# Kernel optimization log

Hardware: AMD Instinct MI355X
Metric: run time of the kernel (lower is better)

## Reference

```python
import jax, jax.numpy as jnp
import numpy as np

SHIFTS = 1
WINDOW_SIZES = (4, 8, 16)
BN_EPS = 1e-5


def _calc_attn_path(x, ws, shifts):
    # x: (b, H, W, 2c) with channels laid out as (qv=2, c)
    b, H, W, c2 = x.shape
    c = c2 // 2
    if shifts > 0:
        x = jnp.roll(x, shift=(-ws // 2, -ws // 2), axis=(1, 2))
    h, w = H // ws, W // ws
    # 'b (h dh) (w dw) (qv c) -> qv (b h w) (dh dw c)'
    qv = x.reshape(b, h, ws, w, ws, 2, c).transpose(5, 0, 1, 3, 2, 4, 6)
    qv = qv.reshape(2, b * h * w, ws * ws * c)
    q, v = qv[0], qv[1]                       # (N, D), N = b*h*w windows, D = ws*ws*c
    atn = jax.nn.softmax(q @ q.T, axis=-1)    # (N, N) attention across windows (as in source)
    y = atn @ v                               # (N, D)
    # '(b h w) (dh dw c) -> b (h dh) (w dw) c'
    y = y.reshape(b, h, w, ws, ws, c).transpose(0, 1, 3, 2, 4, 5).reshape(b, H, W, c)
    if shifts > 0:
        y = jnp.roll(y, shift=(ws // 2, ws // 2), axis=(1, 2))
    return y, atn


def setup_inputs() -> dict:
    key = jax.random.key(0)
    ks = jax.random.split(key, 3)
    B, H, W, C = 4, 128, 128, 180
    inputs = jax.random.normal(ks[0], (B, H, W, C), jnp.float32)
    conv1_w = jax.random.normal(ks[1], (1, 1, C, 2 * C), jnp.float32) * 0.05
    conv1_b = jnp.zeros((2 * C,), jnp.float32)
    bn_scale = jnp.ones((2 * C,), jnp.float32)
    bn_bias = jnp.zeros((2 * C,), jnp.float32)
    conv2_w = jax.random.normal(ks[2], (1, 1, C, C), jnp.float32) * 0.05
    conv2_b = jnp.zeros((C,), jnp.float32)
    return {"inputs": inputs, "conv1_w": conv1_w, "conv1_b": conv1_b,
            "bn_scale": bn_scale, "bn_bias": bn_bias,
            "conv2_w": conv2_w, "conv2_b": conv2_b}


def reference(inputs, conv1_w, conv1_b, bn_scale, bn_bias, conv2_w, conv2_b):
    # 1x1 conv to 2*C channels (calc_attn=True)
    x = jnp.einsum('bhwc,cd->bhwd', inputs, conv1_w[0, 0]) + conv1_b
    # BatchNorm in training mode (batch statistics)
    mean = x.mean(axis=(0, 1, 2))
    var = x.var(axis=(0, 1, 2))
    x = (x - mean) * jax.lax.rsqrt(var + BN_EPS) * bn_scale + bn_bias
    xs = jnp.split(x, 3, axis=-1)             # three groups of 2*C/3 channels
    ys, attns = [], []
    for ws, xi in zip(WINDOW_SIZES, xs):
        y, a = _calc_attn_path(xi, ws, SHIFTS)
        ys.append(y)
        attns.append(a)
    y = jnp.concatenate(ys, axis=-1)          # back to C channels
    y = jnp.einsum('bhwc,cd->bhwd', y, conv2_w[0, 0]) + conv2_b
    return (y, *attns)
```

## Files before the change

kernel.cpp:

```cpp
#include <hip/hip_runtime.h>

typedef unsigned short u16;
typedef __bf16 bf16x8 __attribute__((ext_vector_type(8)));
typedef float f32x4 __attribute__((ext_vector_type(4)));
typedef u16 u16x4 __attribute__((ext_vector_type(4)));
typedef u16 u16x8 __attribute__((ext_vector_type(8)));

__device__ __forceinline__ u16 f2bf(float v) {
    unsigned u = __float_as_uint(v);
    unsigned r = (u + 0x7fffu + ((u >> 16) & 1u)) >> 16;
    return (u16)r;
}
__device__ __forceinline__ float bf2f(u16 u) { return __uint_as_float(((unsigned)u) << 16); }

__device__ __forceinline__ void async_cp16(const u16* g, u16* l) {
    __builtin_amdgcn_global_load_lds((const __attribute__((address_space(1))) unsigned int*)g,
                                     (__attribute__((address_space(3))) unsigned int*)l, 16, 0, 0);
}

__global__ __launch_bounds__(256) void gemm_f32(
    const u16* __restrict__ A, const u16* __restrict__ B,
    float* __restrict__ C, const float* __restrict__ bias,
    int K, int ldc, int n_store)
{
    __shared__ char smem[16384];
    u16* As = (u16*)smem;
    u16* Bs = (u16*)(smem + 8192);
    const int tid = threadIdx.x;
    const int lane = tid & 63;
    const int wave = tid >> 6;
    const int wm = wave >> 1, wn = wave & 1;
    const long m0 = (long)blockIdx.y * 128;
    const long n0 = (long)blockIdx.x * 128;

    f32x4 acc[4][4] = {};
    const int lrow = tid >> 2;
    const int lk = (tid & 3) << 3;
    const u16* Ag = A + (m0 + lrow) * (long)K + lk;
    const u16* Bg = B + (n0 + lrow) * (long)K + lk;
    u16* Asl = As + tid * 8;
    u16* Bsl = Bs + tid * 8;
    const long K64 = (long)64 * K;

    for (int k0 = 0; k0 < K; k0 += 32) {
        async_cp16(Ag + k0, Asl);
        async_cp16(Ag + k0 + K64, Asl + 2048);
        async_cp16(Bg + k0, Bsl);
        async_cp16(Bg + k0 + K64, Bsl + 2048);
        __syncthreads();
        bf16x8 af[4], bg[4];
        const int ro = (lane & 15) * 32 + ((lane >> 4) << 3);
#pragma unroll
        for (int i = 0; i < 4; i++) af[i] = *(const bf16x8*)(As + (wm * 64 + i * 16) * 32 + ro);
#pragma unroll
        for (int j = 0; j < 4; j++) bg[j] = *(const bf16x8*)(Bs + (wn * 64 + j * 16) * 32 + ro);
#pragma unroll
        for (int i = 0; i < 4; i++)
#pragma unroll
            for (int j = 0; j < 4; j++)
                acc[i][j] = __builtin_amdgcn_mfma_f32_16x16x32_bf16(af[i], bg[j], acc[i][j], 0, 0, 0);
        __syncthreads();
    }

    float bv[4];
#pragma unroll
    for (int j = 0; j < 4; j++) bv[j] = bias[n0 + wn * 64 + j * 16 + (lane & 15)];

    float* Cs = (float*)smem;
    for (int c = 0; c < 4; c++) {
        __syncthreads();
        if (wm == (c >> 1)) {
#pragma unroll
            for (int ii = 0; ii < 2; ii++) {
                const int i = (c & 1) * 2 + ii;
#pragma unroll
                for (int j = 0; j < 4; j++)
#pragma unroll
                    for (int r = 0; r < 4; r++) {
                        const int lr = ii * 16 + ((lane >> 4) << 2) + r;
                        Cs[lr * 128 + wn * 64 + j * 16 + (lane & 15)] = acc[i][j][r] + bv[j];
                    }
            }
        }
        __syncthreads();
        const int lr = tid >> 3;
        const int cg = (tid & 7) * 16;
        const long rowg = m0 + c * 32 + lr;
#pragma unroll
        for (int e = 0; e < 4; e++) {
            const int colg = cg + e * 4;
            if ((int)n0 + colg < n_store)
                *(f32x4*)(C + rowg * (long)ldc + n0 + colg) = *(const f32x4*)(Cs + lr * 128 + colg);
        }
    }
}

__global__ __launch_bounds__(256) void conv1_gemm(
    const float* __restrict__ A, const u16* __restrict__ B,
    u16* __restrict__ C, const float* __restrict__ bias)
{
    __shared__ char smem[16384];
    u16* As = (u16*)smem;
    u16* Bs = (u16*)(smem + 8192);
    const int tid = threadIdx.x;
    const int lane = tid & 63;
    const int wave = tid >> 6;
    const int wm = wave >> 1, wn = wave & 1;
    const long m0 = (long)blockIdx.y * 128;
    const long n0 = (long)blockIdx.x * 128;

    f32x4 acc[4][4] = {};
    const int lrow = tid >> 2;
    const int lk = (tid & 3) << 3;
    const float* Ar0 = A + (m0 + lrow) * 180L;
    const float* Ar1 = Ar0 + 64 * 180L;
    const u16* Bg = B + (n0 + lrow) * 192L + lk;
    u16* Asl = As + tid * 8;
    u16* Bsl = Bs + tid * 8;

#pragma unroll
    for (int k0 = 0; k0 < 192; k0 += 32) {
        const int gk = k0 + lk;
        u16x8 oa, ob;
        if (gk + 8 <= 180) {
            f32x4 a0 = *(const f32x4*)(Ar0 + gk), a1 = *(const f32x4*)(Ar0 + gk + 4);
            f32x4 b0 = *(const f32x4*)(Ar1 + gk), b1 = *(const f32x4*)(Ar1 + gk + 4);
#pragma unroll
            for (int c = 0; c < 4; c++) {
                oa[c] = f2bf(a0[c]); oa[4 + c] = f2bf(a1[c]);
                ob[c] = f2bf(b0[c]); ob[4 + c] = f2bf(b1[c]);
            }
        } else if (gk < 180) {
            f32x4 a0 = *(const f32x4*)(Ar0 + gk);
            f32x4 b0 = *(const f32x4*)(Ar1 + gk);
#pragma unroll
            for (int c = 0; c < 4; c++) {
                oa[c] = f2bf(a0[c]); oa[4 + c] = 0;
                ob[c] = f2bf(b0[c]); ob[4 + c] = 0;
            }
        } else {
#pragma unroll
            for (int c = 0; c < 8; c++) { oa[c] = 0; ob[c] = 0; }
        }
        *(u16x8*)Asl = oa;
        *(u16x8*)(Asl + 2048) = ob;
        async_cp16(Bg + k0, Bsl);
        async_cp16(Bg + k0 + 64 * 192, Bsl + 2048);
        __syncthreads();
        bf16x8 af[4], bg[4];
        const int ro = (lane & 15) * 32 + ((lane >> 4) << 3);
#pragma unroll
        for (int i = 0; i < 4; i++) af[i] = *(const bf16x8*)(As + (wm * 64 + i * 16) * 32 + ro);
#pragma unroll
        for (int j = 0; j < 4; j++) bg[j] = *(const bf16x8*)(Bs + (wn * 64 + j * 16) * 32 + ro);
#pragma unroll
        for (int i = 0; i < 4; i++)
#pragma unroll
            for (int j = 0; j < 4; j++)
                acc[i][j] = __builtin_amdgcn_mfma_f32_16x16x32_bf16(af[i], bg[j], acc[i][j], 0, 0, 0);
        __syncthreads();
    }

    float bv[4];
#pragma unroll
    for (int j = 0; j < 4; j++) bv[j] = bias[n0 + wn * 64 + j * 16 + (lane & 15)];

    u16* Cs = (u16*)smem;
    for (int c = 0; c < 2; c++) {
        __syncthreads();
        if (wm == c) {
#pragma unroll
            for (int i = 0; i < 4; i++)
#pragma unroll
                for (int j = 0; j < 4; j++)
#pragma unroll
                    for (int r = 0; r < 4; r++) {
                        const int lr = i * 16 + ((lane >> 4) << 2) + r;
                        Cs[lr * 128 + wn * 64 + j * 16 + (lane & 15)] = f2bf(acc[i][j][r] + bv[j]);
                    }
        }
        __syncthreads();
        const int lr = tid >> 2;
        const int cg = (tid & 3) * 32;
        const long rowg = m0 + c * 64 + lr;
#pragma unroll
        for (int e = 0; e < 4; e++) {
            const int colg = cg + e * 8;
            *(u16x8*)(C + rowg * 384L + n0 + colg) = *(const u16x8*)(Cs + lr * 128 + colg);
        }
    }
}

__global__ __launch_bounds__(256) void qq_all(
    const u16* __restrict__ q0, const u16* __restrict__ q1, const u16* __restrict__ q2,
    float* __restrict__ S0, float* __restrict__ pG1, float* __restrict__ pG2)
{
    __shared__ char smem[16384];
    u16* As = (u16*)smem;
    u16* Bs = (u16*)(smem + 8192);
    const int bid = blockIdx.x;
    int seg, local;
    if (bid < 1024) { seg = 0; local = bid; }
    else if (bid < 1536) { seg = 1; local = bid - 1024; }
    else { seg = 2; local = bid - 1536; }
    const int tX = seg == 0 ? 32 : (seg == 1 ? 8 : 2);
    const int tt = tX * tX;
    const int K = seg == 0 ? 1024 : (seg == 1 ? 3840 : 15360);
    const int Ksplit = seg == 0 ? 1024 : (seg == 1 ? 480 : 256);
    const int N = seg == 0 ? 4096 : (seg == 1 ? 1024 : 256);
    const u16* A = seg == 0 ? q0 : (seg == 1 ? q1 : q2);
    float* outP = seg == 0 ? S0 : (seg == 1 ? pG1 : pG2);
    const int z = local / tt;
    const int rem = local - z * tt;
    const int bx = rem % tX;
    const int by = rem / tX;

    const int tid = threadIdx.x;
    const int lane = tid & 63;
    const int wave = tid >> 6;
    const int wm = wave >> 1, wn = wave & 1;
    const long m0 = (long)by * 128;
    const long n0 = (long)bx * 128;
    const int kbeg = z * Ksplit;

    f32x4 acc[4][4] = {};
    const int lrow = tid >> 2;
    const int lk = (tid & 3) << 3;
    const u16* Ag = A + (m0 + lrow) * (long)K + lk;
    const u16* Bg = A + (n0 + lrow) * (long)K + lk;
    u16* Asl = As + tid * 8;
    u16* Bsl = Bs + tid * 8;
    const long K64 = (long)64 * K;

    for (int k0 = kbeg; k0 < kbeg + Ksplit; k0 += 32) {
        async_cp16(Ag + k0, Asl);
        async_cp16(Ag + k0 + K64, Asl + 2048);
        async_cp16(Bg + k0, Bsl);
        async_cp16(Bg + k0 + K64, Bsl + 2048);
        __syncthreads();
        bf16x8 af[4], bg[4];
        const int ro = (lane & 15) * 32 + ((lane >> 4) << 3);
#pragma unroll
        for (int i = 0; i < 4; i++) af[i] = *(const bf16x8*)(As + (wm * 64 + i * 16) * 32 + ro);
#pragma unroll
        for (int j = 0; j < 4; j++) bg[j] = *(const bf16x8*)(Bs + (wn * 64 + j * 16) * 32 + ro);
#pragma unroll
        for (int i = 0; i < 4; i++)
#pragma unroll
            for (int j = 0; j < 4; j++)
                acc[i][j] = __builtin_amdgcn_mfma_f32_16x16x32_bf16(af[i], bg[j], acc[i][j], 0, 0, 0);
        __syncthreads();
    }

    float* Pz = outP + (long)z * N * N;
    float* Cs = (float*)smem;
    for (int c = 0; c < 4; c++) {
        __syncthreads();
        if (wm == (c >> 1)) {
#pragma unroll
            for (int ii = 0; ii < 2; ii++) {
                const int i = (c & 1) * 2 + ii;
#pragma unroll
                for (int j = 0; j < 4; j++)
#pragma unroll
                    for (int r = 0; r < 4; r++) {
                        const int lr = ii * 16 + ((lane >> 4) << 2) + r;
                        Cs[lr * 128 + wn * 64 + j * 16 + (lane & 15)] = acc[i][j][r];
                    }
            }
        }
        __syncthreads();
        const int lr = tid >> 3;
        const int cg = (tid & 7) * 16;
        const long rowg = m0 + c * 32 + lr;
#pragma unroll
        for (int e = 0; e < 4; e++) {
            const int colg = cg + e * 4;
            *(f32x4*)(Pz + rowg * (long)N + n0 + colg) = *(const f32x4*)(Cs + lr * 128 + colg);
        }
    }
}

__global__ __launch_bounds__(256) void pv_all(
    const u16* __restrict__ a0, const u16* __restrict__ a1, const u16* __restrict__ a2,
    const u16* __restrict__ vt0, const u16* __restrict__ vt1, const u16* __restrict__ vt2,
    u16* __restrict__ Ysp)
{
    __shared__ char smem[16384];
    u16* As = (u16*)smem;
    u16* Bs = (u16*)(smem + 8192);
    const int bid = blockIdx.x;
    int seg, local;
    if (bid < 256) { seg = 0; local = bid; }
    else if (bid < 496) { seg = 1; local = bid - 256; }
    else { seg = 2; local = bid - 496; }
    const int tX = seg == 0 ? 8 : (seg == 1 ? 30 : 120);
    const int K = seg == 0 ? 4096 : (seg == 1 ? 1024 : 256);
    const int D = seg == 0 ? 960 : (seg == 1 ? 3840 : 15360);
    const int l2ws = 2 + seg;
    const int l2wc = 5 - seg;
    const u16* A = seg == 0 ? a0 : (seg == 1 ? a1 : a2);
    const u16* B = seg == 0 ? vt0 : (seg == 1 ? vt1 : vt2);
    const int bx = local % tX;
    const int by = local / tX;

    const int tid = threadIdx.x;
    const int lane = tid & 63;
    const int wave = tid >> 6;
    const int wm = wave >> 1, wn = wave & 1;
    const long m0 = (long)by * 128;
    const long n0 = (long)bx * 128;

    f32x4 acc[4][4] = {};
    const int lrow = tid >> 2;
    const int lk = (tid & 3) << 3;
    const u16* Ag = A + (m0 + lrow) * (long)K + lk;
    const u16* Bg = B + (n0 + lrow) * (long)K + lk;
    u16* Asl = As + tid * 8;
    u16* Bsl = Bs + tid * 8;
    const long K64 = (long)64 * K;

    for (int k0 = 0; k0 < K; k0 += 32) {
        async_cp16(Ag + k0, Asl);
        async_cp16(Ag + k0 + K64, Asl + 2048);
        async_cp16(Bg + k0, Bsl);
        async_cp16(Bg + k0 + K64, Bsl + 2048);
        __syncthreads();
        bf16x8 af[4], bg[4];
        const int ro = (lane & 15) * 32 + ((lane >> 4) << 3);
#pragma unroll
        for (int i = 0; i < 4; i++) af[i] = *(const bf16x8*)(As + (wm * 64 + i * 16) * 32 + ro);
#pragma unroll
        for (int j = 0; j < 4; j++) bg[j] = *(const bf16x8*)(Bs + (wn * 64 + j * 16) * 32 + ro);
#pragma unroll
        for (int i = 0; i < 4; i++)
#pragma unroll
            for (int j = 0; j < 4; j++)
                acc[i][j] = __builtin_amdgcn_mfma_f32_16x16x32_bf16(af[i], bg[j], acc[i][j], 0, 0, 0);
        __syncthreads();
    }

    u16* Cs = (u16*)smem;
    const int wcm = (1 << l2wc) - 1;
    const int wsm = (1 << l2ws) - 1;
    const int sh = 1 << (l2ws - 1);
    for (int c = 0; c < 2; c++) {
        __syncthreads();
        if (wm == c) {
#pragma unroll
            for (int i = 0; i < 4; i++)
#pragma unroll
                for (int j = 0; j < 4; j++)
#pragma unroll
                    for (int r = 0; r < 4; r++) {
                        const int lr = i * 16 + ((lane >> 4) << 2) + r;
                        Cs[lr * 128 + wn * 64 + j * 16 + (lane & 15)] = f2bf(acc[i][j][r]);
                    }
        }
        __syncthreads();
        const int lr = tid >> 2;
        const int cgbase = (tid & 3) * 32;
        const int n = (int)m0 + c * 64 + lr;
        const int wi = n & wcm;
        const int hi = (n >> l2wc) & wcm;
        const int bb = n >> (2 * l2wc);
        const int rowb = (hi << l2ws) + sh;
        const int colb = (wi << l2ws) + sh;
        const long bbase = (long)bb * 128 * 128 * 192 + 60 * seg;
#pragma unroll
        for (int e = 0; e < 8; e++) {
            const int colg = cgbase + e * 4;
            const int d = (int)n0 + colg;
            if (d < D) {
                const int cc = d % 60;
                const int pp = d / 60;
                const int dh = pp >> l2ws;
                const int dw = pp & wsm;
                const int row = (rowb + dh) & 127;
                const int col = (colb + dw) & 127;
                *(u16x4*)(Ysp + bbase + ((long)row * 128 + col) * 192 + cc) =
                    *(const u16x4*)(Cs + lr * 128 + colg);
            }
        }
    }
}

__global__ __launch_bounds__(256) void zero_pad(u16* __restrict__ Ysp)
{
    const long r = (long)blockIdx.x * 256 + threadIdx.x;
    u16* p = Ysp + r * 192 + 180;
    const u16x4 z = {0, 0, 0, 0};
    *(u16x4*)(p) = z;
    *(u16x4*)(p + 4) = z;
    *(u16x4*)(p + 8) = z;
}

__global__ __launch_bounds__(192) void prep_all(
    const float* __restrict__ W1, const float* __restrict__ W2,
    const float* __restrict__ b1, const float* __restrict__ b2,
    u16* __restrict__ W1t, u16* __restrict__ W2t,
    float* __restrict__ b1p, float* __restrict__ b2p, float* __restrict__ accum)
{
    const int bid = blockIdx.x;
    const int t = threadIdx.x;
    if (bid < 384) {
        W1t[bid * 192 + t] = (bid < 360 && t < 180) ? f2bf(W1[t * 360 + bid]) : (u16)0;
    } else if (bid < 640) {
        const int n = bid - 384;
        W2t[n * 192 + t] = (n < 180 && t < 180) ? f2bf(W2[t * 180 + n]) : (u16)0;
    } else {
#pragma unroll
        for (int j = 0; j < 4; j++) {
            const int i = t + 192 * j;
            if (i < 384) b1p[i] = (i < 360) ? b1[i] : 0.0f;
            else if (i < 640) { const int k = i - 384; b2p[k] = (k < 180) ? b2[k] : 0.0f; }
            if (i < 768) accum[i] = 0.0f;
        }
    }
}

__global__ __launch_bounds__(384) void bn_stats(const u16* __restrict__ x, float* __restrict__ accum)
{
    const int ch = threadIdx.x;
    const long base = (long)blockIdx.x * 256 * 384;
    float s = 0.0f, s2 = 0.0f;
    for (int r = 0; r < 256; r++) {
        const float v = bf2f(x[base + (long)r * 384 + ch]);
        s += v; s2 += v * v;
    }
    atomicAdd(&accum[ch], s);
    atomicAdd(&accum[384 + ch], s2);
}

__global__ __launch_bounds__(256) void gather_all(
    const u16* __restrict__ x, const float* __restrict__ accum,
    const float* __restrict__ bns, const float* __restrict__ bnb,
    u16* __restrict__ q0, u16* __restrict__ q1, u16* __restrict__ q2,
    u16* __restrict__ vt0, u16* __restrict__ vt1, u16* __restrict__ vt2)
{
    __shared__ u16 t[64][65];
    const int bid = blockIdx.x;
    int seg, local;
    if (bid < 1024) { seg = 0; local = bid; }
    else if (bid < 1984) { seg = 1; local = bid - 1024; }
    else { seg = 2; local = bid - 1984; }
    const int tX = seg == 0 ? 16 : (seg == 1 ? 60 : 240);
    const int N = seg == 0 ? 4096 : (seg == 1 ? 1024 : 256);
    const int D = seg == 0 ? 960 : (seg == 1 ? 3840 : 15360);
    const int Dp = seg == 0 ? 1024 : (seg == 1 ? 3840 : 15360);
    const int l2ws = 2 + seg;
    const int l2wc = 5 - seg;
    u16* q = seg == 0 ? q0 : (seg == 1 ? q1 : q2);
    u16* vt = seg == 0 ? vt0 : (seg == 1 ? vt1 : vt2);
    const int bx = local % tX;
    const int by = local / tX;

    const int d0 = bx * 64;
    const int n0 = by * 64;
    const int tc = threadIdx.x & 63;
    const int tr = threadIdx.x >> 6;

    const int d = d0 + tc;
    const int sh = 1 << (l2ws - 1);
    const int cc = d % 60;
    const int pp = d / 60;
    const int dh = pp >> l2ws;
    const int dw = pp & ((1 << l2ws) - 1);
    const int wcm = (1 << l2wc) - 1;
    const int ch = 120 * seg + cc;
    const float m_q = accum[ch] * (1.0f / 65536.0f);
    const float v_q = accum[384 + ch] * (1.0f / 65536.0f) - m_q * m_q;
    const float seq = bns[ch] * rsqrtf(v_q + 1e-5f);
    const float beq = bnb[ch] - m_q * seq;
    const float m_v = accum[ch + 60] * (1.0f / 65536.0f);
    const float v_v = accum[384 + ch + 60] * (1.0f / 65536.0f) - m_v * m_v;
    const float sev = bns[ch + 60] * rsqrtf(v_v + 1e-5f);
    const float bev = bnb[ch + 60] - m_v * sev;
    const bool valid = d < D;

#pragma unroll 4
    for (int i = 0; i < 16; i++) {
        const int n = n0 + i * 4 + tr;
        const int wi = n & wcm;
        const int hi = (n >> l2wc) & wcm;
        const int b = n >> (2 * l2wc);
        const int row = ((hi << l2ws) + dh + sh) & 127;
        const int col = ((wi << l2ws) + dw + sh) & 127;
        const long src = ((long)((b << 7) + row) * 128 + col) * 384 + ch;
        const float xq = bf2f(x[src]);
        const float xv = bf2f(x[src + 60]);
        q[(long)n * Dp + d] = valid ? f2bf(seq * xq + beq) : (u16)0;
        t[tc][i * 4 + tr] = f2bf(sev * xv + bev);
    }
    __syncthreads();
#pragma unroll 4
    for (int i = 0; i < 16; i++) {
        const int dd = i * 4 + tr;
        vt[(long)(d0 + dd) * N + n0 + tc] = t[dd][tc];
    }
}

template <int VPT>
__device__ __forceinline__ void softmax_body(
    const float* __restrict__ P, int nsplit, long MN, int rowi,
    float* __restrict__ S, u16* __restrict__ Sb)
{
    const int N = VPT * 256;
    const long base = (long)rowi * N;
    float v[VPT];
    float mx = -3.0e38f;
#pragma unroll
    for (int i = 0; i < VPT; i++) {
        const long idx = base + i * 256 + threadIdx.x;
        float val = P[idx];
        for (int z = 1; z < nsplit; z++) val += P[(long)z * MN + idx];
        v[i] = val; mx = fmaxf(mx, val);
    }
#pragma unroll
    for (int o = 32; o > 0; o >>= 1) mx = fmaxf(mx, __shfl_down(mx, o, 64));
    __shared__ float redm[4];
    if ((threadIdx.x & 63) == 0) redm[threadIdx.x >> 6] = mx;
    __syncthreads();
    mx = fmaxf(fmaxf(redm[0], redm[1]), fmaxf(redm[2], redm[3]));
    float s = 0.0f;
#pragma unroll
    for (int i = 0; i < VPT; i++) { v[i] = __expf(v[i] - mx); s += v[i]; }
#pragma unroll
    for (int o = 32; o > 0; o >>= 1) s += __shfl_down(s, o, 64);
    __shared__ float reds[4];
    if ((threadIdx.x & 63) == 0) reds[threadIdx.x >> 6] = s;
    __syncthreads();
    s = reds[0] + reds[1] + reds[2] + reds[3];
    const float inv = 1.0f / s;
#pragma unroll
    for (int i = 0; i < VPT; i++) {
        const float r = v[i] * inv;
        const long idx = base + i * 256 + threadIdx.x;
        S[idx] = r;
        Sb[idx] = f2bf(r);
    }
}

__global__ __launch_bounds__(256) void softmax_all(
    float* __restrict__ S0, const float* __restrict__ pG1, const float* __restrict__ pG2,
    float* __restrict__ out1, float* __restrict__ out2,
    u16* __restrict__ ab0, u16* __restrict__ ab1, u16* __restrict__ ab2)
{
    const int r = blockIdx.x;
    if (r < 4096)      softmax_body<16>(S0, 1, 16777216L, r, S0, ab0);
    else if (r < 5120) softmax_body<4>(pG1, 8, 1048576L, r - 4096, out1, ab1);
    else               softmax_body<1>(pG2, 60, 65536L, r - 5120, out2, ab2);
}

extern "C" void kernel_launch(void* const* d_in, const int* in_sizes, int n_in,
                              void* d_out, int out_size, void* d_ws, size_t ws_size,
                              hipStream_t stream)
{
    const float* in_x = (const float*)d_in[0];
    const float* w1  = (const float*)d_in[1];
    const float* b1  = (const float*)d_in[2];
    const float* bns = (const float*)d_in[3];
    const float* bnb = (const float*)d_in[4];
    const float* w2  = (const float*)d_in[5];
    const float* b2  = (const float*)d_in[6];
    float* out = (float*)d_out;

    char* w = (char*)d_ws;
    u16* atnb0 = (u16*)w;
    size_t off = 33554432;
    u16* x = (u16*)(w + off);
    float* pG1 = (float*)(w + off);
    float* pG2 = (float*)(w + off + 33554432);
    u16* Ysp = (u16*)(w + off);
    off += 50331648;
    u16* W1t = (u16*)(w + off);  off += 147456;
    u16* W2t = (u16*)(w + off);  off += 98304;
    float* b1p = (float*)(w + off);   off += 4096;
    float* b2p = (float*)(w + off);   off += 4096;
    float* accum = (float*)(w + off); off += 4096;
    u16* q0 = (u16*)(w + off);  off += 8388608;
    u16* q1 = (u16*)(w + off);  off += 7864320;
    u16* q2 = (u16*)(w + off);  off += 7864320;
    u16* vt0 = (u16*)(w + off); off += 8388608;
    u16* vt1 = (u16*)(w + off); off += 7864320;
    u16* vt2 = (u16*)(w + off); off += 7864320;
    u16* atnb1 = (u16*)(w + off); off += 2097152;
    u16* atnb2 = (u16*)(w + off); off += 131072;

    float* S0 = out + 11796480L;
    float* S1 = out + 28573696L;
    float* S2 = out + 29622272L;

    prep_all<<<641, 192, 0, stream>>>(w1, w2, b1, b2, W1t, W2t, b1p, b2p, accum);
    conv1_gemm<<<dim3(3, 512), 256, 0, stream>>>(in_x, W1t, x, b1p);
    bn_stats<<<256, 384, 0, stream>>>(x, accum);
    gather_all<<<2944, 256, 0, stream>>>(x, accum, bns, bnb, q0, q1, q2, vt0, vt1, vt2);
    qq_all<<<1776, 256, 0, stream>>>(q0, q1, q2, S0, pG1, pG2);
    softmax_all<<<5376, 256, 0, stream>>>(S0, pG1, pG2, S1, S2, atnb0, atnb1, atnb2);
    zero_pad<<<256, 256, 0, stream>>>(Ysp);
    pv_all<<<736, 256, 0, stream>>>(atnb0, atnb1, atnb2, vt0, vt1, vt2, Ysp);
    gemm_f32<<<dim3(2, 512), 256, 0, stream>>>(Ysp, W2t, out, b2p, 192, 180, 180);
}
```

Baseline: 485.4 us.

## Split-K the window-4 PV GEMM into two halves with a separate reduce-scatter kernel

The segment-0 PV GEMM (K=4096, only 256 tiles) is split along K into two halves, doubling its block count so the long-K tiles no longer dominate the tail of the kernel. Each half writes fp32 partials into reused workspace (the q0 buffer and part of the Ysp region), and a new kernel sums them, converts to bf16 and scatters into the shifted Ysp layout. It also adds an occupancy hint to launch_bounds. The cost is extra fp32 partial traffic and one additional kernel launch, plus care needed that the reused buffers do not overlap live data.

```diff
diff --git a/kernel.cpp b/kernel.cpp
--- a/kernel.cpp
+++ b/kernel.cpp
@@ -281,21 +281,22 @@
     }
 }
 
-__global__ __launch_bounds__(256) void pv_all(
+__global__ __launch_bounds__(256, 4) void pv_all(
     const u16* __restrict__ a0, const u16* __restrict__ a1, const u16* __restrict__ a2,
     const u16* __restrict__ vt0, const u16* __restrict__ vt1, const u16* __restrict__ vt2,
-    u16* __restrict__ Ysp)
+    u16* __restrict__ Ysp, float* __restrict__ pP0, float* __restrict__ pP1)
 {
     __shared__ char smem[16384];
     u16* As = (u16*)smem;
     u16* Bs = (u16*)(smem + 8192);
     const int bid = blockIdx.x;
-    int seg, local;
-    if (bid < 256) { seg = 0; local = bid; }
-    else if (bid < 496) { seg = 1; local = bid - 256; }
-    else { seg = 2; local = bid - 496; }
+    int seg, local, z = 0;
+    if (bid < 512) { seg = 0; z = bid >> 8; local = bid & 255; }
+    else if (bid < 752) { seg = 1; local = bid - 512; }
+    else { seg = 2; local = bid - 752; }
     const int tX = seg == 0 ? 8 : (seg == 1 ? 30 : 120);
     const int K = seg == 0 ? 4096 : (seg == 1 ? 1024 : 256);
+    const int Ksplit = seg == 0 ? 2048 : K;
     const int D = seg == 0 ? 960 : (seg == 1 ? 3840 : 15360);
     const int l2ws = 2 + seg;
     const int l2wc = 5 - seg;
@@ -310,6 +311,7 @@
     const int wm = wave >> 1, wn = wave & 1;
     const long m0 = (long)by * 128;
     const long n0 = (long)bx * 128;
+    const int kbeg = z * Ksplit;
 
     f32x4 acc[4][4] = {};
     const int lrow = tid >> 2;
@@ -320,7 +322,7 @@
     u16* Bsl = Bs + tid * 8;
     const long K64 = (long)64 * K;
 
-    for (int k0 = 0; k0 < K; k0 += 32) {
+    for (int k0 = kbeg; k0 < kbeg + Ksplit; k0 += 32) {
         async_cp16(Ag + k0, Asl);
         async_cp16(Ag + k0 + K64, Asl + 2048);
         async_cp16(Bg + k0, Bsl);
@@ -338,6 +340,37 @@
             for (int j = 0; j < 4; j++)
                 acc[i][j] = __builtin_amdgcn_mfma_f32_16x16x32_bf16(af[i], bg[j], acc[i][j], 0, 0, 0);
         __syncthreads();
+    }
+
+    if (seg == 0) {
+        float* Pz = (z == 0) ? pP0 : pP1;
+        float* Cs = (float*)smem;
+        for (int c = 0; c < 4; c++) {
+            __syncthreads();
+            if (wm == (c >> 1)) {
+#pragma unroll
+                for (int ii = 0; ii < 2; ii++) {
+                    const int i = (c & 1) * 2 + ii;
+#pragma unroll
+                    for (int j = 0; j < 4; j++)
+#pragma unroll
+                        for (int r = 0; r < 4; r++) {
+                            const int lr = ii * 16 + ((lane >> 4) << 2) + r;
+                            Cs[lr * 128 + wn * 64 + j * 16 + (lane & 15)] = acc[i][j][r];
+                        }
+                }
+            }
+            __syncthreads();
+            const int lr = tid >> 3;
+            const int cg = (tid & 7) * 16;
+            const long rowg = m0 + c * 32 + lr;
+#pragma unroll
+            for (int e = 0; e < 4; e++) {
+                const int colg = cg + e * 4;
+                *(f32x4*)(Pz + rowg * 1024L + n0 + colg) = *(const f32x4*)(Cs + lr * 128 + colg);
+            }
+        }
+        return;
     }
 
     u16* Cs = (u16*)smem;
@@ -383,6 +416,29 @@
             }
         }
     }
+}
+
+__global__ __launch_bounds__(256) void reduce_scatter_g0(
+    const float* __restrict__ pP0, const float* __restrict__ pP1, u16* __restrict__ Ysp)
+{
+    const int n = blockIdx.x;
+    const int d = threadIdx.x * 4;
+    if (d >= 960) return;
+    const long i = (long)n * 1024 + d;
+    f32x4 s = *(const f32x4*)(pP0 + i) + *(const f32x4*)(pP1 + i);
+    const int cc = d % 60;
+    const int pp = d / 60;
+    const int dh = pp >> 2;
+    const int dw = pp & 3;
+    const int wi = n & 31;
+    const int hi = (n >> 5) & 31;
+    const int b = n >> 10;
+    const int row = ((hi << 2) + dh + 2) & 127;
+    const int col = ((wi << 2) + dw + 2) & 127;
+    u16x4 o;
+#pragma unroll
+    for (int c = 0; c < 4; c++) o[c] = f2bf(s[c]);
+    *(u16x4*)(Ysp + ((long)((b << 7) + row) * 128 + col) * 192 + cc) = o;
 }
 
 __global__ __launch_bounds__(256) void zero_pad(u16* __restrict__ Ysp)
@@ -572,6 +628,7 @@
     float* pG1 = (float*)(w + off);
     float* pG2 = (float*)(w + off + 33554432);
     u16* Ysp = (u16*)(w + off);
+    float* pP1 = (float*)(w + off + 25165824);
     off += 50331648;
     u16* W1t = (u16*)(w + off);  off += 147456;
     u16* W2t = (u16*)(w + off);  off += 98304;
@@ -586,6 +643,7 @@
     u16* vt2 = (u16*)(w + off); off += 7864320;
     u16* atnb1 = (u16*)(w + off); off += 2097152;
     u16* atnb2 = (u16*)(w + off); off += 131072;
+    float* pP0 = (float*)q0;
 
     float* S0 = out + 11796480L;
     float* S1 = out + 28573696L;
@@ -598,6 +656,7 @@
     qq_all<<<1776, 256, 0, stream>>>(q0, q1, q2, S0, pG1, pG2);
     softmax_all<<<5376, 256, 0, stream>>>(S0, pG1, pG2, S1, S2, atnb0, atnb1, atnb2);
     zero_pad<<<256, 256, 0, stream>>>(Ysp);
-    pv_all<<<736, 256, 0, stream>>>(atnb0, atnb1, atnb2, vt0, vt1, vt2, Ysp);
+    pv_all<<<992, 256, 0, stream>>>(atnb0, atnb1, atnb2, vt0, vt1, vt2, Ysp, pP0, pP1);
+    reduce_scatter_g0<<<4096, 256, 0, stream>>>(pP0, pP1, Ysp);
     gemm_f32<<<dim3(2, 512), 256, 0, stream>>>(Ysp, W2t, out, b2p, 192, 180, 180);
 }
```

Result: faster. 467.8 us (-3.6%).
